# Performance work log

Hardware: AMD Instinct MI355X
Metric: run time of the kernel (lower is better)

The kernel has to match this reference:

```python
import jax, jax.numpy as jnp
import numpy as np

REG_MAX = 16
NUM_CLASSES = 1
NUM_KPTS = 17
TOPK = 13
EPS = 1e-9

OKS_SIGMAS = np.array([0.026,0.025,0.025,0.035,0.035,0.079,0.079,0.072,0.072,0.062,0.062,0.107,0.107,0.087,0.087,0.089,0.089], np.float32)


def _bce(logits, target):
    # stable binary_cross_entropy_with_logits, reduction='none'
    return jnp.maximum(logits, 0.0) - logits * target + jnp.log1p(jnp.exp(-jnp.abs(logits)))


def _pairwise_iou(gt, pred):
    # gt [B,n,4], pred [B,L,4] -> iou [B,n,L]
    g = gt[:, :, None, :]
    p = pred[:, None, :, :]
    inter_w = jnp.clip(jnp.minimum(g[..., 2], p[..., 2]) - jnp.maximum(g[..., 0], p[..., 0]), 0.0)
    inter_h = jnp.clip(jnp.minimum(g[..., 3], p[..., 3]) - jnp.maximum(g[..., 1], p[..., 1]), 0.0)
    inter = inter_w * inter_h
    ag = (g[..., 2] - g[..., 0]) * (g[..., 3] - g[..., 1])
    ap = (p[..., 2] - p[..., 0]) * (p[..., 3] - p[..., 1])
    return inter / (ag + ap - inter + EPS)


def _assign(pred_scores_sig, pred_bboxes, anchor_points, gt_class, gt_bboxes, pad_gt_mask):
    # TaskAlignedAssigner(topk=13, alpha=1.0, beta=6.0)
    B, n, _ = gt_bboxes.shape
    L = pred_bboxes.shape[1]
    ious = _pairwise_iou(gt_bboxes, pred_bboxes)                                  # [B,n,L]
    idx = jnp.broadcast_to(gt_class, (B, n, L))
    cls = jnp.take_along_axis(jnp.swapaxes(pred_scores_sig, 1, 2), idx, axis=1)   # [B,n,L]
    metrics = cls * ious ** 6.0                                                   # alpha=1, beta=6
    ap = anchor_points[None, None, :, :]
    in_gt = ((ap[..., 0] - gt_bboxes[:, :, None, 0] > EPS)
             & (ap[..., 1] - gt_bboxes[:, :, None, 1] > EPS)
             & (gt_bboxes[:, :, None, 2] - ap[..., 0] > EPS)
             & (gt_bboxes[:, :, None, 3] - ap[..., 1] > EPS)).astype(metrics.dtype)
    _, topk_idx = jax.lax.top_k(metrics * in_gt, TOPK)                            # [B,n,K]
    topk_idx = jnp.where(pad_gt_mask > 0, topk_idx, 0)
    is_in_topk = jax.nn.one_hot(topk_idx, L, dtype=metrics.dtype).sum(-2)
    is_in_topk = jnp.where(is_in_topk > 1, 0.0, is_in_topk)
    mask_pos = is_in_topk * in_gt * pad_gt_mask                                   # [B,n,L]
    # resolve anchors assigned to multiple gts: keep gt with max iou
    is_max_iou = jnp.swapaxes(jax.nn.one_hot(ious.argmax(axis=1), n, dtype=metrics.dtype), 1, 2)
    mask_pos = jnp.where(mask_pos.sum(1, keepdims=True) > 1, is_max_iou, mask_pos)
    pos = mask_pos.sum(1) > 0                                                     # [B,L]
    assigned_gt_index = mask_pos.argmax(1)                                        # [B,L]
    bix = jnp.arange(B)[:, None]
    assigned_labels = jnp.where(pos, gt_class[bix, assigned_gt_index, 0], NUM_CLASSES)
    assigned_bboxes = gt_bboxes[bix, assigned_gt_index]                           # [B,L,4]
    one_hot_lbl = jax.nn.one_hot(assigned_labels, NUM_CLASSES + 1, dtype=metrics.dtype)[..., :NUM_CLASSES]
    # rescale alignment metrics by per-gt max iou / max metric
    m = metrics * mask_pos
    m = m / (m.max(-1, keepdims=True) + EPS) * (ious * mask_pos).max(-1, keepdims=True)
    assigned_scores = one_hot_lbl * m.max(1)[..., None]                           # [B,L,1]
    return assigned_labels, assigned_bboxes, assigned_scores, assigned_gt_index, pos


def _bbox_decode(anchor_points_s, pred_distri):
    B, L, _ = pred_distri.shape
    prob = jax.nn.softmax(pred_distri.reshape(B, L, 4, REG_MAX + 1), axis=-1)
    dist = prob @ jnp.arange(REG_MAX + 1, dtype=prob.dtype)                       # DFL projection
    return jnp.concatenate([anchor_points_s - dist[..., :2], anchor_points_s + dist[..., 2:]], -1)


def _giou(pb, gb):
    inter_w = jnp.clip(jnp.minimum(pb[..., 2], gb[..., 2]) - jnp.maximum(pb[..., 0], gb[..., 0]), 0.0)
    inter_h = jnp.clip(jnp.minimum(pb[..., 3], gb[..., 3]) - jnp.maximum(pb[..., 1], gb[..., 1]), 0.0)
    inter = inter_w * inter_h
    a1 = (pb[..., 2] - pb[..., 0]) * (pb[..., 3] - pb[..., 1])
    a2 = (gb[..., 2] - gb[..., 0]) * (gb[..., 3] - gb[..., 1])
    union = a1 + a2 - inter + EPS
    iou = inter / union
    cw = jnp.maximum(pb[..., 2], gb[..., 2]) - jnp.minimum(pb[..., 0], gb[..., 0])
    ch = jnp.maximum(pb[..., 3], gb[..., 3]) - jnp.minimum(pb[..., 1], gb[..., 1])
    area_c = cw * ch + EPS
    return 1.0 - (iou - (area_c - union) / area_c)


def _df_loss(pred_dist, target):
    # pred_dist [B,L,4,reg_max+1], target [B,L,4] in [0, reg_max-0.01]
    tl = jnp.floor(target).astype(jnp.int32)
    wl = (tl.astype(target.dtype) + 1.0) - target
    logp = jax.nn.log_softmax(pred_dist, -1)
    ll = -jnp.take_along_axis(logp, tl[..., None], -1)[..., 0]
    lr = -jnp.take_along_axis(logp, (tl + 1)[..., None], -1)[..., 0]
    return (ll * wl + lr * (1.0 - wl)).mean(-1)                                   # [B,L]


def _forward(pred_scores, pred_distri, pred_pose_logits, anchor_points, stride_tensor,
             gt_bboxes, pad_gt_mask, gt_poses, oks_sigmas, gt_class):
    B, L, _ = pred_scores.shape
    anchor_points_s = anchor_points / stride_tensor
    pred_bboxes = _bbox_decode(anchor_points_s, pred_distri)
    sgd = jax.lax.stop_gradient
    assigned_labels, assigned_bboxes, assigned_scores, assigned_gt_index, pos = _assign(
        sgd(jax.nn.sigmoid(pred_scores)), sgd(pred_bboxes * stride_tensor), anchor_points,
        gt_class, gt_bboxes, pad_gt_mask)
    assigned_bboxes = assigned_bboxes / stride_tensor
    # focal classification loss (alpha=-1 -> no alpha weighting, gamma=2)
    w = jnp.abs(jax.nn.sigmoid(pred_scores) - assigned_scores) ** 2
    ass_sum = jnp.maximum(assigned_scores.sum(), 1.0)
    loss_cls = (w * _bce(pred_scores, assigned_scores)).sum() / ass_sum
    posf = pos.astype(pred_scores.dtype)
    bbox_w = assigned_scores.sum(-1) * posf                                        # [B,L]
    loss_iou = (_giou(pred_bboxes, assigned_bboxes) * bbox_w).sum() / ass_sum
    ltrb = jnp.clip(jnp.concatenate([anchor_points_s - assigned_bboxes[..., :2],
                                     assigned_bboxes[..., 2:] - anchor_points_s], -1),
                    0.0, REG_MAX - 0.01)
    loss_dfl = (_df_loss(pred_distri.reshape(B, L, 4, REG_MAX + 1), ltrb) * bbox_w).sum() / ass_sum
    bix = jnp.arange(B)[:, None]
    kpts = gt_poses[bix, assigned_gt_index]                                        # [B,L,J,3]
    gt_xy = kpts[..., :2] / stride_tensor[None, :, None, :]
    pred_xy = pred_pose_logits[..., :2] + anchor_points_s[None, :, None, :]
    d = ((pred_xy - gt_xy) ** 2).sum(-1)                                           # [B,L,J]
    kmf = ((kpts[..., 2] != 0) & pos[..., None]).astype(d.dtype)
    area = ((assigned_bboxes[..., 2] - assigned_bboxes[..., 0])
            * (assigned_bboxes[..., 3] - assigned_bboxes[..., 1]))[..., None]
    e = d / (2.0 * oks_sigmas[None, None, :]) ** 2 / (area + EPS) / 2.0
    n_pos_kpts = jnp.maximum(posf.sum() * NUM_KPTS, 1.0)
    factor = n_pos_kpts / (kmf.sum() + EPS)
    loss_pose_reg = factor * ((1.0 - jnp.exp(-e)) * kmf).sum() / n_pos_kpts
    loss_pose_cls = (_bce(pred_pose_logits[..., 2], kmf) * posf[..., None]).sum() / n_pos_kpts
    loss = 1.0 * loss_cls + 2.5 * loss_iou + 0.5 * loss_dfl + 1.0 * loss_pose_cls + 1.0 * loss_pose_reg
    log_losses = jnp.stack([loss_cls, loss_iou, loss_dfl, loss_pose_cls, loss_pose_reg, loss])
    return loss, log_losses


def _make_anchors():
    pts, strides = [], []
    for s in (8, 16, 32):
        g = 640 // s
        xs = (np.arange(g, dtype=np.float32) + 0.5) * s
        yv, xv = np.meshgrid(xs, xs, indexing='ij')
        pts.append(np.stack([xv.ravel(), yv.ravel()], -1))
        strides.append(np.full((g * g, 1), s, np.float32))
    return jnp.asarray(np.concatenate(pts)), jnp.asarray(np.concatenate(strides))


def setup_inputs() -> dict:
    B, N, J, L = 16, 32, 17, 8400
    key = jax.random.key(0)
    ks = jax.random.split(key, 8)
    anchor_points, stride_tensor = _make_anchors()
    x1y1 = jax.random.uniform(ks[0], (B, N, 2), minval=0.0, maxval=480.0)
    wh = jax.random.uniform(ks[1], (B, N, 2), minval=32.0, maxval=160.0)
    gt_bboxes = jnp.concatenate([x1y1, x1y1 + wh], -1)
    pad_gt_mask = jnp.broadcast_to((jnp.arange(N)[None, :, None] < 24), (B, N, 1)).astype(jnp.float32)
    gt_class = jnp.zeros((B, N, 1), jnp.int32)
    ctr = x1y1 + wh / 2.0
    kxy = ctr[:, :, None, :] + jax.random.normal(ks[2], (B, N, J, 2)) * wh[:, :, None, :] * 0.2
    vis = jax.random.randint(ks[3], (B, N, J), 0, 3).astype(jnp.float32)
    gt_poses = jnp.concatenate([kxy, vis[..., None]], -1)
    pred_scores = jax.random.normal(ks[4], (B, L, 1)) * 0.5 - 2.0
    pred_distri = jax.random.normal(ks[5], (B, L, 4 * (REG_MAX + 1)))
    pred_pose_logits = jax.random.normal(ks[6], (B, L, J, 3))
    return {'pred_scores': pred_scores, 'pred_distri': pred_distri,
            'pred_pose_logits': pred_pose_logits, 'anchor_points': anchor_points,
            'stride_tensor': stride_tensor, 'gt_bboxes': gt_bboxes,
            'pad_gt_mask': pad_gt_mask, 'gt_poses': gt_poses,
            'oks_sigmas': jnp.asarray(OKS_SIGMAS), 'gt_class': gt_class}


def reference(pred_scores, pred_distri, pred_pose_logits, anchor_points, stride_tensor,
              gt_bboxes, pad_gt_mask, gt_poses, oks_sigmas, gt_class):
    return _forward(pred_scores, pred_distri, pred_pose_logits, anchor_points, stride_tensor,
                    gt_bboxes, pad_gt_mask, gt_poses, oks_sigmas, gt_class)
```

## Files before the change

### kernel.cpp

```cpp
#include <hip/hip_runtime.h>
#include <cstddef>

#define EPS 1e-9f
#define REG_MAX 16
#define TOPK 13
#define MAXL 8400
#define TPB 1024
#define CAP 1024
#define LSLOT 16

__device__ __forceinline__ float sigmoidf(float x){ return 1.0f/(1.0f+expf(-x)); }
__device__ __forceinline__ float bcef(float l, float t){
    return fmaxf(l,0.0f) - l*t + log1pf(expf(-fabsf(l)));
}
__device__ __forceinline__ float pow6f(float x){ float x2=x*x; return x2*x2*x2; }

__global__ void k_decode(const float* __restrict__ pred_scores,
                         const float* __restrict__ pred_distri,
                         const float* __restrict__ anchor_points,
                         const float* __restrict__ stride_t,
                         float* __restrict__ pred_bboxes,
                         float* __restrict__ sig,
                         int B, int L)
{
    int idx = blockIdx.x*blockDim.x + threadIdx.x;
    if (idx >= B*L) return;
    int l = idx % L;
    float v[68];
    const float4* pd4 = (const float4*)(pred_distri + (size_t)idx*68);
    #pragma unroll
    for (int i=0;i<17;i++){ float4 q = pd4[i]; v[4*i]=q.x; v[4*i+1]=q.y; v[4*i+2]=q.z; v[4*i+3]=q.w; }
    float dist[4];
    #pragma unroll
    for (int s=0;s<4;s++){
        float m = -1e30f;
        #pragma unroll
        for (int i=0;i<=REG_MAX;i++) m = fmaxf(m, v[s*17+i]);
        float sum=0.f, ws=0.f;
        #pragma unroll
        for (int i=0;i<=REG_MAX;i++){ float e = expf(v[s*17+i]-m); sum+=e; ws += e*(float)i; }
        dist[s] = ws/sum;
    }
    float st = stride_t[l];
    float ax = anchor_points[2*l]/st, ay = anchor_points[2*l+1]/st;
    float4 box = make_float4(ax-dist[0], ay-dist[1], ax+dist[2], ay+dist[3]);
    ((float4*)pred_bboxes)[idx] = box;
    sig[idx] = sigmoidf(pred_scores[idx]);
}

__global__ void k_assign_topk(const float* __restrict__ pred_bboxes,
                              const float* __restrict__ sig,
                              const float* __restrict__ anchor_points,
                              const float* __restrict__ stride_t,
                              const float* __restrict__ gt_bboxes,
                              const float* __restrict__ pad_mask,
                              float* __restrict__ ious,
                              unsigned char* __restrict__ maskA,
                              int B,int N,int L)
{
    __shared__ int   scnt;
    __shared__ float sval[CAP];
    __shared__ int   sidx[CAP];
    int bn = blockIdx.x; int b = bn / N; int n = bn % N;
    const float4 gb = ((const float4*)gt_bboxes)[bn];
    float gx1=gb.x, gy1=gb.y, gx2=gb.z, gy2=gb.w;
    float ag = (gx2-gx1)*(gy2-gy1);
    int tid = threadIdx.x;
    bool valid = pad_mask[bn] > 0.f;
    if (tid==0) scnt=0;
    __syncthreads();

    for (int l=tid; l<L; l+=TPB){
        float4 pb = ((const float4*)pred_bboxes)[b*L + l];
        float st = stride_t[l];
        float p0 = pb.x*st, p1 = pb.y*st, p2 = pb.z*st, p3 = pb.w*st;
        float iw = fmaxf(fminf(gx2,p2)-fmaxf(gx1,p0), 0.f);
        float ih = fmaxf(fminf(gy2,p3)-fmaxf(gy1,p1), 0.f);
        float inter = iw*ih;
        float ap = (p2-p0)*(p3-p1);
        float iou = inter/(ag+ap-inter+EPS);
        ious[(size_t)bn*L + l] = iou;
        if (valid){
            float apx = anchor_points[2*l], apy = anchor_points[2*l+1];
            bool ing = (apx-gx1>EPS)&&(apy-gy1>EPS)&&(gx2-apx>EPS)&&(gy2-apy>EPS);
            if (ing){
                float v = sig[b*L+l]*pow6f(iou);
                int slot = atomicAdd(&scnt, 1);
                if (slot < CAP){ sval[slot]=v; sidx[slot]=l; }
            }
        }
    }
    __syncthreads();
    if (!valid) return;
    int cnt = scnt < CAP ? scnt : CAP;

    if (cnt <= TOPK){
        for (int i=tid; i<cnt; i+=TPB)
            maskA[(size_t)(b*L + sidx[i])*N + n] = 1;
        return;
    }
    if (tid >= 64) return;
    float lv[LSLOT]; int li[LSLOT];
    #pragma unroll
    for (int k=0;k<LSLOT;k++){ lv[k]=-1.f; li[k]=0x7fffffff; }
    for (int i=tid; i<cnt; i+=64){
        float cv = sval[i]; int ci = sidx[i];
        #pragma unroll
        for (int k=0;k<LSLOT;k++){
            bool better = (cv>lv[k]) || (cv==lv[k] && ci<li[k]);
            if (better){
                float tv=lv[k]; lv[k]=cv; cv=tv;
                int   ti=li[k]; li[k]=ci; ci=ti;
            }
        }
    }
    for (int r=0;r<TOPK;r++){
        float bv=lv[0]; int bl=li[0];
        #pragma unroll
        for (int off=32; off>0; off>>=1){
            float ov = __shfl_xor(bv, off);
            int   oi = __shfl_xor(bl, off);
            if (ov>bv || (ov==bv && oi<bl)){ bv=ov; bl=oi; }
        }
        if (li[0]==bl){
            maskA[(size_t)(b*L + bl)*N + n] = 1;
            #pragma unroll
            for (int k=0;k<LSLOT-1;k++){ lv[k]=lv[k+1]; li[k]=li[k+1]; }
            lv[LSLOT-1]=-1.f; li[LSLOT-1]=0x7fffffff;
        }
    }
}

__global__ void k_resolve(const unsigned char* __restrict__ maskA,
                          const float* __restrict__ ious,
                          unsigned int* __restrict__ words,
                          int B,int N,int L)
{
    int idx = blockIdx.x*blockDim.x + threadIdx.x;
    if (idx >= B*L) return;
    int b = idx / L, l = idx % L;
    const uint4* row4 = (const uint4*)(maskA + (size_t)idx*N);
    uint4 r0 = row4[0], r1 = row4[1];
    unsigned int wd[8] = {r0.x,r0.y,r0.z,r0.w,r1.x,r1.y,r1.z,r1.w};
    unsigned int w=0; int cnt=0;
    #pragma unroll
    for (int q=0;q<8;q++){
        unsigned int v = wd[q];
        #pragma unroll
        for (int c=0;c<4;c++){
            if ((v>>(8*c))&0xffu){ w |= 1u<<(q*4+c); cnt++; }
        }
    }
    if (cnt > 1){
        float bv=-1e30f; int bbest=0;
        for (int n=0;n<N;n++){
            float vv = ious[((size_t)(b*N+n))*L + l];
            if (vv > bv){ bv=vv; bbest=n; }
        }
        w = 1u<<bbest;
    }
    words[idx] = w;
}

__global__ void k_rowmax(const unsigned int* __restrict__ words,
                         const float* __restrict__ ious,
                         const float* __restrict__ sig,
                         float* __restrict__ rowmax_m,
                         float* __restrict__ rowmax_iou,
                         int B,int N,int L)
{
    __shared__ float srm[16], srio[16];
    int bn = blockIdx.x; int b = bn/N; int n = bn%N;
    int tid=threadIdx.x;
    float mm=0.f, mi=0.f;
    for (int l=tid;l<L;l+=TPB){
        unsigned int w = words[b*L+l];
        if ((w>>n)&1u){
            float iou = ious[(size_t)bn*L+l];
            float met = sig[b*L+l]*pow6f(iou);
            mm = fmaxf(mm, met); mi = fmaxf(mi, iou);
        }
    }
    #pragma unroll
    for (int off=32; off>0; off>>=1){
        mm = fmaxf(mm, __shfl_xor(mm, off));
        mi = fmaxf(mi, __shfl_xor(mi, off));
    }
    if ((tid&63)==0){ srm[tid>>6]=mm; srio[tid>>6]=mi; }
    __syncthreads();
    if (tid==0){
        float fm=srm[0], fi=srio[0];
        #pragma unroll
        for (int w2=1;w2<16;w2++){ fm=fmaxf(fm,srm[w2]); fi=fmaxf(fi,srio[w2]); }
        rowmax_m[bn]=fm; rowmax_iou[bn]=fi;
    }
}

__global__ void k_loss(const float* __restrict__ pred_scores,
                       const float* __restrict__ pred_distri,
                       const float* __restrict__ pose_logits,
                       const float* __restrict__ anchor_points,
                       const float* __restrict__ stride_t,
                       const float* __restrict__ gt_bboxes,
                       const float* __restrict__ gt_poses,
                       const float* __restrict__ sigmas,
                       const int*   __restrict__ gt_class,
                       const float* __restrict__ pred_bboxes,
                       const float* __restrict__ sig,
                       const float* __restrict__ ious,
                       const unsigned int* __restrict__ words,
                       const float* __restrict__ rowmax_m,
                       const float* __restrict__ rowmax_iou,
                       float* __restrict__ partials,
                       int B,int N,int L,int J)
{
    int idx = blockIdx.x*blockDim.x + threadIdx.x;
    float a_score=0, a_cls=0, a_giou=0, a_dfl=0, a_pos=0, a_kmf=0, a_preg=0, a_pcls=0;
    if (idx < B*L){
        int b=idx/L, l=idx%L;
        unsigned int w = words[idx];
        bool pos = (w!=0u);
        int gi = pos ? (__ffs(w)-1) : 0;
        float score = 0.f;
        unsigned int ww=w;
        while (ww){
            int n = __ffs(ww)-1; ww &= ww-1u;
            float iou = ious[((size_t)(b*N+n))*L + l];
            float met = sig[idx]*pow6f(iou);
            float vv = met/(rowmax_m[b*N+n]+EPS)*rowmax_iou[b*N+n];
            score = fmaxf(score, vv);
        }
        int acls = pos ? gt_class[b*N+gi] : 1;
        float assigned = (pos && acls==0) ? score : 0.f;
        float logit = pred_scores[idx];
        float sg = sig[idx];
        float wg = sg - assigned; wg *= wg;
        a_cls = wg * bcef(logit, assigned);
        a_score = assigned;
        if (pos){
            a_pos = 1.f;
            float st = stride_t[l];
            const float4 gb4 = ((const float4*)gt_bboxes)[b*N+gi];
            float ab0=gb4.x/st, ab1=gb4.y/st, ab2=gb4.z/st, ab3=gb4.w/st;
            float area = (ab2-ab0)*(ab3-ab1);
            float apx = anchor_points[2*l]/st, apy = anchor_points[2*l+1]/st;
            float bw = assigned;
            if (bw > 0.f){
                float4 pb = ((const float4*)pred_bboxes)[idx];
                float iw = fmaxf(fminf(pb.z,ab2)-fmaxf(pb.x,ab0),0.f);
                float ih = fmaxf(fminf(pb.w,ab3)-fmaxf(pb.y,ab1),0.f);
                float inter=iw*ih;
                float a1=(pb.z-pb.x)*(pb.w-pb.y);
                float a2=(ab2-ab0)*(ab3-ab1);
                float uni=a1+a2-inter+EPS;
                float iou=inter/uni;
                float cw=fmaxf(pb.z,ab2)-fminf(pb.x,ab0);
                float ch=fmaxf(pb.w,ab3)-fminf(pb.y,ab1);
                float ac=cw*ch+EPS;
                float g = 1.f-(iou-(ac-uni)/ac);
                a_giou = g*bw;
                float t4[4] = { apx-ab0, apy-ab1, ab2-apx, ab3-apy };
                const float* pdist = pred_distri + (size_t)idx*68;
                float dfl=0.f;
                #pragma unroll
                for (int s2=0;s2<4;s2++){
                    float tt = fminf(fmaxf(t4[s2],0.f),(float)REG_MAX-0.01f);
                    int tl = (int)floorf(tt);
                    float wl = (float)tl + 1.f - tt;
                    float m=-1e30f;
                    for (int i=0;i<=REG_MAX;i++) m=fmaxf(m,pdist[s2*17+i]);
                    float se=0.f;
                    for (int i=0;i<=REG_MAX;i++) se+=expf(pdist[s2*17+i]-m);
                    float lse = m + logf(se);
                    float ll = -(pdist[s2*17+tl]-lse);
                    float lr = -(pdist[s2*17+tl+1]-lse);
                    dfl += ll*wl + lr*(1.f-wl);
                }
                a_dfl = dfl*0.25f*bw;
            }
            const float* gp = gt_poses + ((size_t)(b*N+gi))*J*3;
            const float* pl = pose_logits + (size_t)idx*J*3;
            for (int j=0;j<J;j++){
                float gx=gp[3*j]/st, gy=gp[3*j+1]/st, vis=gp[3*j+2];
                float px=pl[3*j]+apx, py=pl[3*j+1]+apy, pz=pl[3*j+2];
                float kmf = (vis!=0.f)?1.f:0.f;
                float dx=px-gx, dy=py-gy;
                float d = dx*dx+dy*dy;
                float s2g = 2.f*sigmas[j]; s2g*=s2g;
                float e = d/s2g/(area+EPS)/2.f;
                a_preg += (1.f-expf(-e))*kmf;
                a_kmf  += kmf;
                a_pcls += bcef(pz, kmf);
            }
        }
    }
    float acc[8] = {a_score,a_cls,a_giou,a_dfl,a_pos,a_kmf,a_preg,a_pcls};
    #pragma unroll
    for (int k=0;k<8;k++){
        #pragma unroll
        for (int off=32; off>0; off>>=1) acc[k] += __shfl_xor(acc[k], off);
    }
    __shared__ float wsum[4][8];
    int wid = threadIdx.x>>6;
    if ((threadIdx.x&63)==0){
        #pragma unroll
        for (int k=0;k<8;k++) wsum[wid][k]=acc[k];
    }
    __syncthreads();
    if (threadIdx.x<8){
        float s = wsum[0][threadIdx.x]+wsum[1][threadIdx.x]
                + wsum[2][threadIdx.x]+wsum[3][threadIdx.x];
        partials[(size_t)blockIdx.x*8+threadIdx.x]=s;
    }
}

__global__ void k_final(const float* __restrict__ partials, int nblk, int J,
                        float* __restrict__ out)
{
    __shared__ float red[256][9];
    int tid = threadIdx.x;
    float acc[8] = {0,0,0,0,0,0,0,0};
    for (int i=tid; i<nblk; i+=256){
        const float4* p = (const float4*)(partials + (size_t)i*8);
        float4 a = p[0], b = p[1];
        acc[0]+=a.x; acc[1]+=a.y; acc[2]+=a.z; acc[3]+=a.w;
        acc[4]+=b.x; acc[5]+=b.y; acc[6]+=b.z; acc[7]+=b.w;
    }
    #pragma unroll
    for (int k=0;k<8;k++) red[tid][k]=acc[k];
    __syncthreads();
    for (int s=128;s>0;s>>=1){
        if (tid<s){
            #pragma unroll
            for (int k=0;k<8;k++) red[tid][k]+=red[tid+s][k];
        }
        __syncthreads();
    }
    if (tid==0){
        float ass  = fmaxf(red[0][0],1.f);
        float lcls = red[0][1]/ass;
        float liou = red[0][2]/ass;
        float ldfl = red[0][3]/ass;
        float npk  = fmaxf(red[0][4]*(float)J,1.f);
        float factor = npk/(red[0][5]+EPS);
        float preg = factor*red[0][6]/npk;
        float pcls = red[0][7]/npk;
        float loss = lcls + 2.5f*liou + 0.5f*ldfl + pcls + preg;
        out[0]=loss; out[1]=lcls; out[2]=liou; out[3]=ldfl;
        out[4]=pcls; out[5]=preg; out[6]=loss;
    }
}

extern "C" void kernel_launch(void* const* d_in, const int* in_sizes, int n_in,
                              void* d_out, int out_size, void* d_ws, size_t ws_size,
                              hipStream_t stream)
{
    const float* pred_scores   = (const float*)d_in[0];
    const float* pred_distri   = (const float*)d_in[1];
    const float* pose_logits   = (const float*)d_in[2];
    const float* anchor_points = (const float*)d_in[3];
    const float* stride_t      = (const float*)d_in[4];
    const float* gt_bboxes     = (const float*)d_in[5];
    const float* pad_mask      = (const float*)d_in[6];
    const float* gt_poses      = (const float*)d_in[7];
    const float* sigmas        = (const float*)d_in[8];
    const int*   gt_class      = (const int*)d_in[9];

    int L = in_sizes[3]/2;
    int B = in_sizes[0]/L;
    int N = in_sizes[5]/(B*4);
    int J = in_sizes[8];

    char* ws = (char*)d_ws;
    size_t off=0;
    auto alloc=[&](size_t bytes)->void*{
        size_t cur=off; off += (bytes+255)/256*256; return (void*)(ws+cur);
    };
    float* ious         = (float*)alloc((size_t)B*N*L*4);
    float* pred_bboxes  = (float*)alloc((size_t)B*L*4*4);
    float* sig          = (float*)alloc((size_t)B*L*4);
    unsigned char* maskA= (unsigned char*)alloc((size_t)B*L*N);
    unsigned int* words = (unsigned int*)alloc((size_t)B*L*4);
    float* rowmax_m     = (float*)alloc((size_t)B*N*4);
    float* rowmax_i     = (float*)alloc((size_t)B*N*4);
    int nblk = (B*L+255)/256;
    float* partials     = (float*)alloc((size_t)nblk*8*4);
    (void)ws_size; (void)n_in; (void)out_size;

    hipMemsetAsync(maskA, 0, (size_t)B*L*N, stream);
    k_decode<<<nblk,256,0,stream>>>(pred_scores,pred_distri,anchor_points,stride_t,
                                    pred_bboxes,sig,B,L);
    k_assign_topk<<<B*N,TPB,0,stream>>>(pred_bboxes,sig,anchor_points,stride_t,
                                        gt_bboxes,pad_mask,ious,maskA,B,N,L);
    k_resolve<<<nblk,256,0,stream>>>(maskA,ious,words,B,N,L);
    k_rowmax<<<B*N,TPB,0,stream>>>(words,ious,sig,rowmax_m,rowmax_i,B,N,L);
    k_loss<<<nblk,256,0,stream>>>(pred_scores,pred_distri,pose_logits,anchor_points,
                                  stride_t,gt_bboxes,gt_poses,sigmas,gt_class,
                                  pred_bboxes,sig,ious,words,rowmax_m,rowmax_i,
                                  partials,B,N,L,J);
    k_final<<<1,256,0,stream>>>(partials,nblk,J,(float*)d_out);
}
```

Before: 107.3 us.

## Replace byte mask with atomic bitwords, fold rowmax into resolve, compact positives

The per-anchor byte mask and its memset are replaced by a 32-bit word per anchor set with atomicOr, and the workspace zeroing moves into the decode kernel. The separate rowmax kernel is removed: resolve now computes per-GT maxima with float-as-uint atomicMax and appends positive anchors to a compacted list. The loss is split into a light dense kernel for classification terms and a sparse kernel that runs box, DFL and pose terms only over the compacted positive anchors. This is meant to cut launches, memory passes and divergent per-anchor work, at the cost of atomic contention and a loss-pos grid sized for the worst case that mostly exits early.

```diff
diff --git a/kernel.cpp b/kernel.cpp
--- a/kernel.cpp
+++ b/kernel.cpp
@@ -21,10 +21,17 @@
                          const float* __restrict__ stride_t,
                          float* __restrict__ pred_bboxes,
                          float* __restrict__ sig,
-                         int B, int L)
+                         unsigned int* __restrict__ words,
+                         unsigned int* __restrict__ rowmax_m,
+                         unsigned int* __restrict__ rowmax_i,
+                         int* __restrict__ pcnt,
+                         int B, int N, int L)
 {
     int idx = blockIdx.x*blockDim.x + threadIdx.x;
     if (idx >= B*L) return;
+    if (idx < B*N){ rowmax_m[idx]=0u; rowmax_i[idx]=0u; }
+    if (idx == 0) *pcnt = 0;
+    words[idx] = 0u;
     int l = idx % L;
     float v[68];
     const float4* pd4 = (const float4*)(pred_distri + (size_t)idx*68);
@@ -55,7 +62,7 @@
                               const float* __restrict__ gt_bboxes,
                               const float* __restrict__ pad_mask,
                               float* __restrict__ ious,
-                              unsigned char* __restrict__ maskA,
+                              unsigned int* __restrict__ words,
                               int B,int N,int L)
 {
     __shared__ int   scnt;
@@ -93,10 +100,11 @@
     __syncthreads();
     if (!valid) return;
     int cnt = scnt < CAP ? scnt : CAP;
+    unsigned int nbit = 1u<<n;
 
     if (cnt <= TOPK){
         for (int i=tid; i<cnt; i+=TPB)
-            maskA[(size_t)(b*L + sidx[i])*N + n] = 1;
+            atomicOr(&words[b*L + sidx[i]], nbit);
         return;
     }
     if (tid >= 64) return;
@@ -123,7 +131,7 @@
             if (ov>bv || (ov==bv && oi<bl)){ bv=ov; bl=oi; }
         }
         if (li[0]==bl){
-            maskA[(size_t)(b*L + bl)*N + n] = 1;
+            atomicOr(&words[b*L + bl], nbit);
             #pragma unroll
             for (int k=0;k<LSLOT-1;k++){ lv[k]=lv[k+1]; li[k]=li[k+1]; }
             lv[LSLOT-1]=-1.f; li[LSLOT-1]=0x7fffffff;
@@ -131,186 +139,200 @@
     }
 }
 
-__global__ void k_resolve(const unsigned char* __restrict__ maskA,
-                          const float* __restrict__ ious,
+__global__ void k_resolve(const float* __restrict__ ious,
+                          const float* __restrict__ sig,
                           unsigned int* __restrict__ words,
+                          unsigned int* __restrict__ rowmax_m,
+                          unsigned int* __restrict__ rowmax_i,
+                          int* __restrict__ poslist,
+                          int* __restrict__ pcnt,
                           int B,int N,int L)
 {
     int idx = blockIdx.x*blockDim.x + threadIdx.x;
     if (idx >= B*L) return;
     int b = idx / L, l = idx % L;
-    const uint4* row4 = (const uint4*)(maskA + (size_t)idx*N);
-    uint4 r0 = row4[0], r1 = row4[1];
-    unsigned int wd[8] = {r0.x,r0.y,r0.z,r0.w,r1.x,r1.y,r1.z,r1.w};
-    unsigned int w=0; int cnt=0;
-    #pragma unroll
-    for (int q=0;q<8;q++){
-        unsigned int v = wd[q];
-        #pragma unroll
-        for (int c=0;c<4;c++){
-            if ((v>>(8*c))&0xffu){ w |= 1u<<(q*4+c); cnt++; }
-        }
-    }
-    if (cnt > 1){
+    unsigned int w = words[idx];
+    if (!w) return;
+    int n;
+    if (__popc(w) > 1){
         float bv=-1e30f; int bbest=0;
-        for (int n=0;n<N;n++){
-            float vv = ious[((size_t)(b*N+n))*L + l];
-            if (vv > bv){ bv=vv; bbest=n; }
-        }
-        w = 1u<<bbest;
-    }
-    words[idx] = w;
-}
-
-__global__ void k_rowmax(const unsigned int* __restrict__ words,
-                         const float* __restrict__ ious,
-                         const float* __restrict__ sig,
-                         float* __restrict__ rowmax_m,
-                         float* __restrict__ rowmax_iou,
-                         int B,int N,int L)
-{
-    __shared__ float srm[16], srio[16];
-    int bn = blockIdx.x; int b = bn/N; int n = bn%N;
-    int tid=threadIdx.x;
-    float mm=0.f, mi=0.f;
-    for (int l=tid;l<L;l+=TPB){
-        unsigned int w = words[b*L+l];
-        if ((w>>n)&1u){
-            float iou = ious[(size_t)bn*L+l];
-            float met = sig[b*L+l]*pow6f(iou);
-            mm = fmaxf(mm, met); mi = fmaxf(mi, iou);
-        }
-    }
-    #pragma unroll
-    for (int off=32; off>0; off>>=1){
-        mm = fmaxf(mm, __shfl_xor(mm, off));
-        mi = fmaxf(mi, __shfl_xor(mi, off));
-    }
-    if ((tid&63)==0){ srm[tid>>6]=mm; srio[tid>>6]=mi; }
-    __syncthreads();
-    if (tid==0){
-        float fm=srm[0], fi=srio[0];
-        #pragma unroll
-        for (int w2=1;w2<16;w2++){ fm=fmaxf(fm,srm[w2]); fi=fmaxf(fi,srio[w2]); }
-        rowmax_m[bn]=fm; rowmax_iou[bn]=fi;
-    }
-}
-
-__global__ void k_loss(const float* __restrict__ pred_scores,
-                       const float* __restrict__ pred_distri,
-                       const float* __restrict__ pose_logits,
-                       const float* __restrict__ anchor_points,
-                       const float* __restrict__ stride_t,
-                       const float* __restrict__ gt_bboxes,
-                       const float* __restrict__ gt_poses,
-                       const float* __restrict__ sigmas,
-                       const int*   __restrict__ gt_class,
-                       const float* __restrict__ pred_bboxes,
-                       const float* __restrict__ sig,
-                       const float* __restrict__ ious,
-                       const unsigned int* __restrict__ words,
-                       const float* __restrict__ rowmax_m,
-                       const float* __restrict__ rowmax_iou,
-                       float* __restrict__ partials,
-                       int B,int N,int L,int J)
+        for (int nn=0;nn<N;nn++){
+            float vv = ious[((size_t)(b*N+nn))*L + l];
+            if (vv > bv){ bv=vv; bbest=nn; }
+        }
+        n = bbest;
+        words[idx] = 1u<<n;
+    } else {
+        n = __ffs(w)-1;
+    }
+    float iou = ious[((size_t)(b*N+n))*L + l];
+    float met = sig[idx]*pow6f(iou);
+    atomicMax(&rowmax_m[b*N+n], __float_as_uint(met));
+    atomicMax(&rowmax_i[b*N+n], __float_as_uint(iou));
+    int slot = atomicAdd(pcnt, 1);
+    poslist[slot] = idx;
+}
+
+__global__ void k_loss_all(const float* __restrict__ pred_scores,
+                           const float* __restrict__ sig,
+                           const float* __restrict__ ious,
+                           const unsigned int* __restrict__ words,
+                           const unsigned int* __restrict__ rowmax_m,
+                           const unsigned int* __restrict__ rowmax_i,
+                           const int* __restrict__ gt_class,
+                           float* __restrict__ partials,
+                           int B,int N,int L)
 {
     int idx = blockIdx.x*blockDim.x + threadIdx.x;
-    float a_score=0, a_cls=0, a_giou=0, a_dfl=0, a_pos=0, a_kmf=0, a_preg=0, a_pcls=0;
+    float a_score=0.f, a_cls=0.f;
     if (idx < B*L){
         int b=idx/L, l=idx%L;
         unsigned int w = words[idx];
-        bool pos = (w!=0u);
-        int gi = pos ? (__ffs(w)-1) : 0;
-        float score = 0.f;
-        unsigned int ww=w;
-        while (ww){
-            int n = __ffs(ww)-1; ww &= ww-1u;
+        float assigned = 0.f;
+        if (w){
+            int n = __ffs(w)-1;
             float iou = ious[((size_t)(b*N+n))*L + l];
             float met = sig[idx]*pow6f(iou);
-            float vv = met/(rowmax_m[b*N+n]+EPS)*rowmax_iou[b*N+n];
-            score = fmaxf(score, vv);
-        }
-        int acls = pos ? gt_class[b*N+gi] : 1;
-        float assigned = (pos && acls==0) ? score : 0.f;
+            float score = met/(__uint_as_float(rowmax_m[b*N+n])+EPS)
+                          *__uint_as_float(rowmax_i[b*N+n]);
+            if (gt_class[b*N+n]==0) assigned = score;
+        }
         float logit = pred_scores[idx];
         float sg = sig[idx];
         float wg = sg - assigned; wg *= wg;
         a_cls = wg * bcef(logit, assigned);
         a_score = assigned;
-        if (pos){
-            a_pos = 1.f;
-            float st = stride_t[l];
-            const float4 gb4 = ((const float4*)gt_bboxes)[b*N+gi];
-            float ab0=gb4.x/st, ab1=gb4.y/st, ab2=gb4.z/st, ab3=gb4.w/st;
-            float area = (ab2-ab0)*(ab3-ab1);
-            float apx = anchor_points[2*l]/st, apy = anchor_points[2*l+1]/st;
-            float bw = assigned;
-            if (bw > 0.f){
-                float4 pb = ((const float4*)pred_bboxes)[idx];
-                float iw = fmaxf(fminf(pb.z,ab2)-fmaxf(pb.x,ab0),0.f);
-                float ih = fmaxf(fminf(pb.w,ab3)-fmaxf(pb.y,ab1),0.f);
-                float inter=iw*ih;
-                float a1=(pb.z-pb.x)*(pb.w-pb.y);
-                float a2=(ab2-ab0)*(ab3-ab1);
-                float uni=a1+a2-inter+EPS;
-                float iou=inter/uni;
-                float cw=fmaxf(pb.z,ab2)-fminf(pb.x,ab0);
-                float ch=fmaxf(pb.w,ab3)-fminf(pb.y,ab1);
-                float ac=cw*ch+EPS;
-                float g = 1.f-(iou-(ac-uni)/ac);
-                a_giou = g*bw;
-                float t4[4] = { apx-ab0, apy-ab1, ab2-apx, ab3-apy };
-                const float* pdist = pred_distri + (size_t)idx*68;
-                float dfl=0.f;
+    }
+    #pragma unroll
+    for (int off=32; off>0; off>>=1){
+        a_score += __shfl_xor(a_score, off);
+        a_cls   += __shfl_xor(a_cls,   off);
+    }
+    __shared__ float ws2[16][2];
+    int wid = threadIdx.x>>6;
+    if ((threadIdx.x&63)==0){ ws2[wid][0]=a_score; ws2[wid][1]=a_cls; }
+    __syncthreads();
+    if (threadIdx.x==0){
+        float s0=0.f, s1=0.f;
+        #pragma unroll
+        for (int i=0;i<16;i++){ s0+=ws2[i][0]; s1+=ws2[i][1]; }
+        float* row = partials + (size_t)blockIdx.x*8;
+        row[0]=s0; row[1]=s1; row[2]=0.f; row[3]=0.f;
+        row[4]=0.f; row[5]=0.f; row[6]=0.f; row[7]=0.f;
+    }
+}
+
+__global__ void k_loss_pos(const float* __restrict__ pred_distri,
+                           const float* __restrict__ pose_logits,
+                           const float* __restrict__ anchor_points,
+                           const float* __restrict__ stride_t,
+                           const float* __restrict__ gt_bboxes,
+                           const float* __restrict__ gt_poses,
+                           const float* __restrict__ sigmas,
+                           const int*   __restrict__ gt_class,
+                           const float* __restrict__ pred_bboxes,
+                           const float* __restrict__ sig,
+                           const float* __restrict__ ious,
+                           const unsigned int* __restrict__ words,
+                           const unsigned int* __restrict__ rowmax_m,
+                           const unsigned int* __restrict__ rowmax_i,
+                           const int* __restrict__ poslist,
+                           const int* __restrict__ pcnt,
+                           float* __restrict__ partials, int rowbase,
+                           int B,int N,int L,int J)
+{
+    int i = blockIdx.x*blockDim.x + threadIdx.x;
+    int cnt = *pcnt;
+    float a_giou=0,a_dfl=0,a_pos=0,a_kmf=0,a_preg=0,a_pcls=0;
+    if (i < cnt){
+        int idx = poslist[i];
+        int b=idx/L, l=idx%L;
+        int n = __ffs(words[idx])-1;
+        float iou0 = ious[((size_t)(b*N+n))*L + l];
+        float met = sig[idx]*pow6f(iou0);
+        float score = met/(__uint_as_float(rowmax_m[b*N+n])+EPS)
+                      *__uint_as_float(rowmax_i[b*N+n]);
+        float assigned = (gt_class[b*N+n]==0) ? score : 0.f;
+        a_pos = 1.f;
+        float st = stride_t[l];
+        const float4 gb4 = ((const float4*)gt_bboxes)[b*N+n];
+        float ab0=gb4.x/st, ab1=gb4.y/st, ab2=gb4.z/st, ab3=gb4.w/st;
+        float area = (ab2-ab0)*(ab3-ab1);
+        float apx = anchor_points[2*l]/st, apy = anchor_points[2*l+1]/st;
+        float bw = assigned;
+        if (bw > 0.f){
+            float4 pb = ((const float4*)pred_bboxes)[idx];
+            float iw = fmaxf(fminf(pb.z,ab2)-fmaxf(pb.x,ab0),0.f);
+            float ih = fmaxf(fminf(pb.w,ab3)-fmaxf(pb.y,ab1),0.f);
+            float inter=iw*ih;
+            float a1=(pb.z-pb.x)*(pb.w-pb.y);
+            float a2=(ab2-ab0)*(ab3-ab1);
+            float uni=a1+a2-inter+EPS;
+            float iou=inter/uni;
+            float cw=fmaxf(pb.z,ab2)-fminf(pb.x,ab0);
+            float ch=fmaxf(pb.w,ab3)-fminf(pb.y,ab1);
+            float ac=cw*ch+EPS;
+            float g = 1.f-(iou-(ac-uni)/ac);
+            a_giou = g*bw;
+            float t4[4] = { apx-ab0, apy-ab1, ab2-apx, ab3-apy };
+            const float* pdist = pred_distri + (size_t)idx*68;
+            const float4* pd4 = (const float4*)pdist;
+            float v[68];
+            #pragma unroll
+            for (int q=0;q<17;q++){ float4 qq=pd4[q]; v[4*q]=qq.x; v[4*q+1]=qq.y; v[4*q+2]=qq.z; v[4*q+3]=qq.w; }
+            float dfl=0.f;
+            #pragma unroll
+            for (int s2=0;s2<4;s2++){
+                float tt = fminf(fmaxf(t4[s2],0.f),(float)REG_MAX-0.01f);
+                int tl = (int)floorf(tt);
+                float wl = (float)tl + 1.f - tt;
+                float m=-1e30f;
                 #pragma unroll
-                for (int s2=0;s2<4;s2++){
-                    float tt = fminf(fmaxf(t4[s2],0.f),(float)REG_MAX-0.01f);
-                    int tl = (int)floorf(tt);
-                    float wl = (float)tl + 1.f - tt;
-                    float m=-1e30f;
-                    for (int i=0;i<=REG_MAX;i++) m=fmaxf(m,pdist[s2*17+i]);
-                    float se=0.f;
-                    for (int i=0;i<=REG_MAX;i++) se+=expf(pdist[s2*17+i]-m);
-                    float lse = m + logf(se);
-                    float ll = -(pdist[s2*17+tl]-lse);
-                    float lr = -(pdist[s2*17+tl+1]-lse);
-                    dfl += ll*wl + lr*(1.f-wl);
-                }
-                a_dfl = dfl*0.25f*bw;
+                for (int q=0;q<=REG_MAX;q++) m=fmaxf(m,v[s2*17+q]);
+                float se=0.f;
+                #pragma unroll
+                for (int q=0;q<=REG_MAX;q++) se+=expf(v[s2*17+q]-m);
+                float lse = m + logf(se);
+                float ll = -(pdist[s2*17+tl]-lse);
+                float lr = -(pdist[s2*17+tl+1]-lse);
+                dfl += ll*wl + lr*(1.f-wl);
             }
-            const float* gp = gt_poses + ((size_t)(b*N+gi))*J*3;
-            const float* pl = pose_logits + (size_t)idx*J*3;
-            for (int j=0;j<J;j++){
-                float gx=gp[3*j]/st, gy=gp[3*j+1]/st, vis=gp[3*j+2];
-                float px=pl[3*j]+apx, py=pl[3*j+1]+apy, pz=pl[3*j+2];
-                float kmf = (vis!=0.f)?1.f:0.f;
-                float dx=px-gx, dy=py-gy;
-                float d = dx*dx+dy*dy;
-                float s2g = 2.f*sigmas[j]; s2g*=s2g;
-                float e = d/s2g/(area+EPS)/2.f;
-                a_preg += (1.f-expf(-e))*kmf;
-                a_kmf  += kmf;
-                a_pcls += bcef(pz, kmf);
-            }
-        }
-    }
-    float acc[8] = {a_score,a_cls,a_giou,a_dfl,a_pos,a_kmf,a_preg,a_pcls};
-    #pragma unroll
-    for (int k=0;k<8;k++){
+            a_dfl = dfl*0.25f*bw;
+        }
+        const float* gp = gt_poses + ((size_t)(b*N+n))*J*3;
+        const float* pl = pose_logits + (size_t)idx*J*3;
+        for (int j=0;j<J;j++){
+            float gx=gp[3*j]/st, gy=gp[3*j+1]/st, vis=gp[3*j+2];
+            float px=pl[3*j]+apx, py=pl[3*j+1]+apy, pz=pl[3*j+2];
+            float kmf = (vis!=0.f)?1.f:0.f;
+            float dx=px-gx, dy=py-gy;
+            float d = dx*dx+dy*dy;
+            float s2g = 2.f*sigmas[j]; s2g*=s2g;
+            float e = d/s2g/(area+EPS)/2.f;
+            a_preg += (1.f-expf(-e))*kmf;
+            a_kmf  += kmf;
+            a_pcls += bcef(pz, kmf);
+        }
+    }
+    float acc[6] = {a_giou,a_dfl,a_pos,a_kmf,a_preg,a_pcls};
+    #pragma unroll
+    for (int k=0;k<6;k++){
         #pragma unroll
         for (int off=32; off>0; off>>=1) acc[k] += __shfl_xor(acc[k], off);
     }
-    __shared__ float wsum[4][8];
+    __shared__ float wsum[4][6];
     int wid = threadIdx.x>>6;
     if ((threadIdx.x&63)==0){
         #pragma unroll
-        for (int k=0;k<8;k++) wsum[wid][k]=acc[k];
+        for (int k=0;k<6;k++) wsum[wid][k]=acc[k];
     }
     __syncthreads();
-    if (threadIdx.x<8){
-        float s = wsum[0][threadIdx.x]+wsum[1][threadIdx.x]
-                + wsum[2][threadIdx.x]+wsum[3][threadIdx.x];
-        partials[(size_t)blockIdx.x*8+threadIdx.x]=s;
+    if (threadIdx.x==0){
+        float* row = partials + (size_t)(rowbase+blockIdx.x)*8;
+        row[0]=0.f; row[1]=0.f;
+        #pragma unroll
+        for (int k=0;k<6;k++)
+            row[2+k]=wsum[0][k]+wsum[1][k]+wsum[2][k]+wsum[3][k];
     }
 }
 
@@ -376,27 +398,35 @@
     auto alloc=[&](size_t bytes)->void*{
         size_t cur=off; off += (bytes+255)/256*256; return (void*)(ws+cur);
     };
-    float* ious         = (float*)alloc((size_t)B*N*L*4);
-    float* pred_bboxes  = (float*)alloc((size_t)B*L*4*4);
-    float* sig          = (float*)alloc((size_t)B*L*4);
-    unsigned char* maskA= (unsigned char*)alloc((size_t)B*L*N);
-    unsigned int* words = (unsigned int*)alloc((size_t)B*L*4);
-    float* rowmax_m     = (float*)alloc((size_t)B*N*4);
-    float* rowmax_i     = (float*)alloc((size_t)B*N*4);
-    int nblk = (B*L+255)/256;
-    float* partials     = (float*)alloc((size_t)nblk*8*4);
+    float* ious           = (float*)alloc((size_t)B*N*L*4);
+    float* pred_bboxes    = (float*)alloc((size_t)B*L*4*4);
+    float* sig            = (float*)alloc((size_t)B*L*4);
+    unsigned int* words   = (unsigned int*)alloc((size_t)B*L*4);
+    unsigned int* rowmax_m= (unsigned int*)alloc((size_t)B*N*4);
+    unsigned int* rowmax_i= (unsigned int*)alloc((size_t)B*N*4);
+    int maxpos = B*N*TOPK;
+    int* poslist          = (int*)alloc((size_t)maxpos*4);
+    int* pcnt             = (int*)alloc(256);
+    int nblk256  = (B*L+255)/256;
+    int nblkA    = (B*L+1023)/1024;
+    int nblkP    = (maxpos+255)/256;
+    float* partials       = (float*)alloc((size_t)(nblkA+nblkP)*8*4);
     (void)ws_size; (void)n_in; (void)out_size;
 
-    hipMemsetAsync(maskA, 0, (size_t)B*L*N, stream);
-    k_decode<<<nblk,256,0,stream>>>(pred_scores,pred_distri,anchor_points,stride_t,
-                                    pred_bboxes,sig,B,L);
+    k_decode<<<nblk256,256,0,stream>>>(pred_scores,pred_distri,anchor_points,
+                                       stride_t,pred_bboxes,sig,
+                                       words,rowmax_m,rowmax_i,pcnt,B,N,L);
     k_assign_topk<<<B*N,TPB,0,stream>>>(pred_bboxes,sig,anchor_points,stride_t,
-                                        gt_bboxes,pad_mask,ious,maskA,B,N,L);
-    k_resolve<<<nblk,256,0,stream>>>(maskA,ious,words,B,N,L);
-    k_rowmax<<<B*N,TPB,0,stream>>>(words,ious,sig,rowmax_m,rowmax_i,B,N,L);
-    k_loss<<<nblk,256,0,stream>>>(pred_scores,pred_distri,pose_logits,anchor_points,
-                                  stride_t,gt_bboxes,gt_poses,sigmas,gt_class,
-                                  pred_bboxes,sig,ious,words,rowmax_m,rowmax_i,
-                                  partials,B,N,L,J);
-    k_final<<<1,256,0,stream>>>(partials,nblk,J,(float*)d_out);
-}
+                                        gt_bboxes,pad_mask,ious,words,B,N,L);
+    k_resolve<<<nblk256,256,0,stream>>>(ious,sig,words,rowmax_m,rowmax_i,
+                                        poslist,pcnt,B,N,L);
+    k_loss_all<<<nblkA,1024,0,stream>>>(pred_scores,sig,ious,words,
+                                        rowmax_m,rowmax_i,gt_class,
+                                        partials,B,N,L);
+    k_loss_pos<<<nblkP,256,0,stream>>>(pred_distri,pose_logits,anchor_points,
+                                       stride_t,gt_bboxes,gt_poses,sigmas,
+                                       gt_class,pred_bboxes,sig,ious,words,
+                                       rowmax_m,rowmax_i,poslist,pcnt,
+                                       partials,nblkA,B,N,L,J);
+    k_final<<<1,256,0,stream>>>(partials,nblkA+nblkP,J,(float*)d_out);
+}
```

After: 96.59 us. -10.0%, faster.
